# Kernel optimization log

Hardware: AMD Instinct MI355X
Metric: run time of the kernel (lower is better)

The kernel has to match this reference:

```python
import jax, jax.numpy as jnp
import numpy as np

N, E, G, H, D = 50000, 800000, 64, 2, 128  # nodes, edges, graphs, heads, out_channels
NEG_SLOPE_ATT = 0.2   # GATv2 default negative_slope
NEG_SLOPE_OUT = 0.01  # torch.nn.LeakyReLU default
BN_EPS = 1e-5


def setup_inputs() -> dict:
    key = jax.random.key(0)
    ks = jax.random.split(key, 12)
    x = jax.random.normal(ks[0], (N, 1), jnp.float32)
    edge_index = jax.random.randint(ks[1], (2, E), 0, N, dtype=jnp.int64)
    edge_attr = jax.random.normal(ks[2], (E,), jnp.float32)
    batch = jnp.sort(jax.random.randint(ks[3], (N,), 0, G, dtype=jnp.int64))
    # GATv2Conv params: lin_l/lin_r: Linear(1, H*D) with bias; lin_edge: Linear(1, H*D) no bias
    Wl = jax.random.normal(ks[4], (1, H * D), jnp.float32) * 0.5
    bl = jax.random.normal(ks[5], (H * D,), jnp.float32) * 0.1
    Wr = jax.random.normal(ks[6], (1, H * D), jnp.float32) * 0.5
    br = jax.random.normal(ks[7], (H * D,), jnp.float32) * 0.1
    We = jax.random.normal(ks[8], (1, H * D), jnp.float32) * 0.5
    att = jax.random.normal(ks[9], (H, D), jnp.float32) * 0.5
    bias = jax.random.normal(ks[10], (D,), jnp.float32) * 0.1
    gamma = jnp.ones((D,), jnp.float32)
    beta = jnp.zeros((D,), jnp.float32)
    return {"x": x, "edge_index": edge_index, "edge_attr": edge_attr, "batch": batch,
            "Wl": Wl, "bl": bl, "Wr": Wr, "br": br, "We": We, "att": att,
            "bias": bias, "gamma": gamma, "beta": beta}


def reference(x, edge_index, edge_attr, batch, Wl, bl, Wr, br, We, att, bias, gamma, beta):
    n = x.shape[0]
    src, dst = edge_index[0], edge_index[1]  # message flows src -> dst
    # node transforms: [N, H, D]
    xl = (x @ Wl + bl).reshape(n, H, D)  # lin_l (source side, also the message value)
    xr = (x @ Wr + br).reshape(n, H, D)  # lin_r (destination side)
    # edge feature embedding: [E, H, D]
    ee = (edge_attr[:, None] @ We).reshape(-1, H, D)
    # GATv2 scoring: leaky_relu(x_j + x_i + e), then dot with attention vector
    m = jax.nn.leaky_relu(xl[src] + xr[dst] + ee, NEG_SLOPE_ATT)  # [E, H, D]
    alpha = jnp.einsum('ehd,hd->eh', m, att)  # [E, H]
    # scatter-softmax over incoming edges per destination node
    amax = jax.ops.segment_max(alpha, dst, num_segments=n)  # [N, H]
    ea = jnp.exp(alpha - amax[dst])
    denom = jax.ops.segment_sum(ea, dst, num_segments=n)
    alpha = ea / (denom[dst] + 1e-16)
    # weighted scatter-add aggregation of x_j
    out = jax.ops.segment_sum(xl[src] * alpha[..., None], dst, num_segments=n)  # [N, H, D]
    out = out.mean(axis=1) + bias  # concat=False -> head average, then conv bias
    # BatchNorm1d in training mode (biased variance over nodes)
    mean = out.mean(axis=0)
    var = ((out - mean) ** 2).mean(axis=0)
    out = (out - mean) * jax.lax.rsqrt(var + BN_EPS) * gamma + beta
    out = jax.nn.leaky_relu(out, NEG_SLOPE_OUT)
    # graph-level scatter_add pooling
    return jax.ops.segment_sum(out, batch, num_segments=G)  # [G, D]
```

## Files before the change

kernel.cpp:

```cpp
#include <hip/hip_runtime.h>
#include <math.h>

#define NN 50000
#define NE 800000
#define NG 64

#define CB    1024
#define NBLK  782
#define NBUCK 196

static_assert(NBLK * CB >= NE, "chunk cover");
static_assert((NBUCK - 1) == (NN - 1) / 256, "bucket count");
static_assert(NE % 4 == 0, "edge unroll");

#define WS_C     0
#define WS_ACC   16
#define WS_BNSUM (WS_ACC + 4*NN)
#define WS_BNSQ  (WS_BNSUM + 128)
#define WS_MOM   WS_BNSUM
#define WS_EX    (WS_BNSQ + 128)
#define WS_TOT   (WS_EX + 272)
#define WS_PK    (WS_TOT + 256)
#define WS_CNT   (WS_PK + 1280)
#define WS_SORT  (WS_CNT + 256*NBLK)
#define WS_END   (WS_SORT + 4*NE)
#define WS_NEED_BYTES ((size_t)WS_END * 4 + 256)

static_assert(((WS_SORT * 4) % 16) == 0, "sort 16B alignment");

typedef float v2f __attribute__((ext_vector_type(2)));

__device__ __forceinline__ v2f pkfma(v2f a, v2f b, v2f c) {
#if __has_builtin(__builtin_elementwise_fma)
  return __builtin_elementwise_fma(a, b, c);
#else
  v2f r; r.x = fmaf(a.x, b.x, c.x); r.y = fmaf(a.y, b.y, c.y); return r;
#endif
}
__device__ __forceinline__ v2f pkabs(v2f a) {
  v2f r; r.x = fabsf(a.x); r.y = fabsf(a.y); return r;
}

#define STEP(wl_, wr_, we_, bb_, at_, xs_, xd_, ae_, acc_)                 \
  { float tt = fmaf(we_, ae_, bb_); tt = fmaf(wr_, xd_, tt);               \
    tt = fmaf(wl_, xs_, tt); acc_ = fmaf(fabsf(tt), at_, acc_); }

#define SMEM_WEIGHTS_DECL                                                  \
  __shared__ __align__(16) float sWl[256], sWr[256], sWe[256], sB[256], sAt[256];

#define SMEM_WEIGHTS_LOAD                                                  \
  { int t_ = threadIdx.x;                                                  \
    sWl[t_] = Wl[t_]; sWr[t_] = Wr[t_]; sWe[t_] = We[t_];                  \
    sB[t_] = bl[t_] + br[t_]; sAt[t_] = att[t_]; }                         \
  __syncthreads();

#define SCORES(xs_, xd_, ae_, accA, accB, out0, out1)                      \
  { float lin0 = fmaf(c0.x, xs_, fmaf(c0.y, xd_, fmaf(c0.z, ae_, c0.w))); \
    out0 = fmaf(0.4f, accA, 0.6f * lin0);                                  \
    float lin1 = fmaf(c1.x, xs_, fmaf(c1.y, xd_, fmaf(c1.z, ae_, c1.w))); \
    out1 = fmaf(0.4f, accB, 0.6f * lin1); }

#define STEP4(c, q0, q1, q2, q3)                                           \
  STEP(wl.c, wr.c, we.c, bb.c, at.c, xs0, xd0, ae0, q0)                    \
  STEP(wl.c, wr.c, we.c, bb.c, at.c, xs1, xd1, ae1, q1)                    \
  STEP(wl.c, wr.c, we.c, bb.c, at.c, xs2, xd2, ae2, q2)                    \
  STEP(wl.c, wr.c, we.c, bb.c, at.c, xs3, xd3, ae3, q3)

#define SCORE_CORE                                                         \
  int4 s4 = *(const int4*)&ei[base];                                       \
  int4 dd4 = *(const int4*)&ei[NE + base];                                 \
  float4 ae4 = *(const float4*)&eattr[base];                               \
  float xs0 = x[s4.x], xs1 = x[s4.y], xs2 = x[s4.z], xs3 = x[s4.w];        \
  float xd0 = x[dd4.x], xd1 = x[dd4.y], xd2 = x[dd4.z], xd3 = x[dd4.w];    \
  float ae0 = ae4.x, ae1 = ae4.y, ae2 = ae4.z, ae3 = ae4.w;

#define SCORE_LOOPS                                                        \
  float a00 = 0.f, a01 = 0.f, a02 = 0.f, a03 = 0.f;                        \
  float a10 = 0.f, a11 = 0.f, a12 = 0.f, a13 = 0.f;                        \
  _Pragma("unroll 2")                                                      \
  for (int j = 0; j < 128; j += 4) {                                       \
    float4 wl = *(const float4*)&sWl[j];                                   \
    float4 wr = *(const float4*)&sWr[j];                                   \
    float4 we = *(const float4*)&sWe[j];                                   \
    float4 bb = *(const float4*)&sB[j];                                    \
    float4 at = *(const float4*)&sAt[j];                                   \
    STEP4(x, a00, a01, a02, a03)                                           \
    STEP4(y, a00, a01, a02, a03)                                           \
    STEP4(z, a00, a01, a02, a03)                                           \
    STEP4(w, a00, a01, a02, a03)                                           \
  }                                                                        \
  _Pragma("unroll 2")                                                      \
  for (int j = 128; j < 256; j += 4) {                                     \
    float4 wl = *(const float4*)&sWl[j];                                   \
    float4 wr = *(const float4*)&sWr[j];                                   \
    float4 we = *(const float4*)&sWe[j];                                   \
    float4 bb = *(const float4*)&sB[j];                                    \
    float4 at = *(const float4*)&sAt[j];                                   \
    STEP4(x, a10, a11, a12, a13)                                           \
    STEP4(y, a10, a11, a12, a13)                                           \
    STEP4(z, a10, a11, a12, a13)                                           \
    STEP4(w, a10, a11, a12, a13)                                           \
  }                                                                        \
  float4 c0 = *(const float4*)&ws[WS_C];                                   \
  float4 c1 = *(const float4*)&ws[WS_C + 4];

extern "C" __global__ __launch_bounds__(256)
void k_hist(const int* __restrict__ ei,
            const float* __restrict__ att, const float* __restrict__ Wl,
            const float* __restrict__ Wr, const float* __restrict__ We,
            const float* __restrict__ bl, const float* __restrict__ br,
            float* __restrict__ ws, float* __restrict__ out)
{
  __shared__ unsigned cnt[256];
  cnt[threadIdx.x] = 0u;
  __syncthreads();
  int base = blockIdx.x * CB + (int)threadIdx.x * 4;
  if (base < NE) {
    int4 a = *(const int4*)&ei[NE + base];
    atomicAdd(&cnt[((unsigned)a.x) >> 8], 1u);
    atomicAdd(&cnt[((unsigned)a.y) >> 8], 1u);
    atomicAdd(&cnt[((unsigned)a.z) >> 8], 1u);
    atomicAdd(&cnt[((unsigned)a.w) >> 8], 1u);
  }
  __syncthreads();
  unsigned* counts = (unsigned*)(ws + WS_CNT);
  counts[(size_t)threadIdx.x * NBLK + blockIdx.x] = cnt[threadIdx.x];
  int gid = blockIdx.x * 256 + (int)threadIdx.x;
  if (gid < NG * 128) out[gid] = 0.f;
  if (gid < 14) ws[WS_MOM + gid] = 0.f;
  if (blockIdx.x == 0) {
    int t = threadIdx.x;
    int jj = (t >> 1) + ((t & 1) << 7);
    ws[WS_PK +        t] = Wl[jj];
    ws[WS_PK +  256 + t] = Wr[jj];
    ws[WS_PK +  512 + t] = We[jj];
    ws[WS_PK +  768 + t] = bl[jj] + br[jj];
    ws[WS_PK + 1024 + t] = att[jj];
    __shared__ float red[4][256];
    float a = att[t];
    red[0][t] = a * Wl[t];
    red[1][t] = a * Wr[t];
    red[2][t] = a * We[t];
    red[3][t] = a * (bl[t] + br[t]);
    __syncthreads();
    if (t < 8) {
      int k = t >> 1, h = t & 1;
      float s = 0.f;
      for (int d = 0; d < 128; ++d) s += red[k][h * 128 + d];
      ws[WS_C + h * 4 + k] = s;
    }
  }
}

extern "C" __global__ __launch_bounds__(256)
void k_scan1(float* __restrict__ ws)
{
  int b = blockIdx.x;
  int t = threadIdx.x;
  unsigned* row = (unsigned*)(ws + WS_CNT) + (size_t)b * NBLK;
  __shared__ unsigned sc[256];
  unsigned carry = 0;
  for (int c = 0; c < NBLK; c += 256) {
    int k = c + t;
    unsigned v = (k < NBLK) ? row[k] : 0u;
    sc[t] = v;
    __syncthreads();
    for (int o = 1; o < 256; o <<= 1) {
      unsigned u = (t >= o) ? sc[t - o] : 0u;
      __syncthreads();
      sc[t] += u;
      __syncthreads();
    }
    unsigned incl = sc[t];
    if (k < NBLK) row[k] = carry + incl - v;
    unsigned total = sc[255];
    __syncthreads();
    carry += total;
  }
  if (t == 0) ((unsigned*)(ws + WS_TOT))[b] = carry;
}

extern "C" __global__ __launch_bounds__(256)
void k_scan2(float* __restrict__ ws)
{
  int b = threadIdx.x;
  unsigned v = ((const unsigned*)(ws + WS_TOT))[b];
  __shared__ unsigned sc[256];
  sc[b] = v;
  __syncthreads();
  for (int o = 1; o < 256; o <<= 1) {
    unsigned u = (b >= o) ? sc[b - o] : 0u;
    __syncthreads();
    sc[b] += u;
    __syncthreads();
  }
  unsigned* ex = (unsigned*)(ws + WS_EX);
  ex[b] = sc[b] - v;
  if (b == 255) ex[256] = sc[b];
}

extern "C" __global__ __launch_bounds__(256, 2)
void k_score(const int* __restrict__ ei, const float* __restrict__ x,
             const float* __restrict__ eattr,
             const float* __restrict__ pk,
             float* __restrict__ ws)
{
  __shared__ unsigned soff[256];
  { int t_ = threadIdx.x;
    const unsigned* counts = (const unsigned*)(ws + WS_CNT);
    const unsigned* ex = (const unsigned*)(ws + WS_EX);
    soff[t_] = ex[t_] + counts[(size_t)t_ * NBLK + blockIdx.x];
  }
  __syncthreads();
  int base = blockIdx.x * CB + (int)threadIdx.x * 4;
  if (base >= NE) return;
  SCORE_CORE
  v2f A0 = {0.f, 0.f}, A1 = A0, A2 = A0, A3 = A0;
#define PKSTEP(wlp, wrp, wep, bbp, atp, xs_, xd_, ae_, acc_)               \
  { v2f tt = pkfma(wep, (v2f){ae_, ae_}, bbp);                             \
    tt = pkfma(wrp, (v2f){xd_, xd_}, tt);                                  \
    tt = pkfma(wlp, (v2f){xs_, xs_}, tt);                                  \
    acc_ = pkfma(pkabs(tt), atp, acc_); }
#define PKSTEP4(wlp, wrp, wep, bbp, atp)                                   \
  PKSTEP(wlp, wrp, wep, bbp, atp, xs0, xd0, ae0, A0)                       \
  PKSTEP(wlp, wrp, wep, bbp, atp, xs1, xd1, ae1, A1)                       \
  PKSTEP(wlp, wrp, wep, bbp, atp, xs2, xd2, ae2, A2)                       \
  PKSTEP(wlp, wrp, wep, bbp, atp, xs3, xd3, ae3, A3)
#pragma unroll 2
  for (int g = 0; g < 64; ++g) {
    float4 wl = *(const float4*)&pk[       4 * g];
    float4 wr = *(const float4*)&pk[ 256 + 4 * g];
    float4 we = *(const float4*)&pk[ 512 + 4 * g];
    float4 bb = *(const float4*)&pk[ 768 + 4 * g];
    float4 at = *(const float4*)&pk[1024 + 4 * g];
    v2f wlA = {wl.x, wl.y}, wrA = {wr.x, wr.y}, weA = {we.x, we.y};
    v2f bbA = {bb.x, bb.y}, atA = {at.x, at.y};
    v2f wlB = {wl.z, wl.w}, wrB = {wr.z, wr.w}, weB = {we.z, we.w};
    v2f bbB = {bb.z, bb.w}, atB = {at.z, at.w};
    PKSTEP4(wlA, wrA, weA, bbA, atA)
    PKSTEP4(wlB, wrB, weB, bbB, atB)
  }
#undef PKSTEP4
#undef PKSTEP
  float4 c0 = *(const float4*)&ws[WS_C];
  float4 c1 = *(const float4*)&ws[WS_C + 4];
  float4* srt = (float4*)(ws + WS_SORT);
  float s0, s1;
#define EPI(i, dv, Acc)                                                    \
  { SCORES(xs##i, xd##i, ae##i, Acc.x, Acc.y, s0, s1)                      \
    unsigned d_ = (unsigned)(dv);                                          \
    unsigned p_ = atomicAdd(&soff[d_ >> 8], 1u);                           \
    srt[p_] = make_float4(__expf(s0), __expf(s1), xs##i, __uint_as_float(d_)); }
  EPI(0, dd4.x, A0) EPI(1, dd4.y, A1)
  EPI(2, dd4.z, A2) EPI(3, dd4.w, A3)
#undef EPI
}

extern "C" __global__ __launch_bounds__(1024)
void k_gather(float* __restrict__ ws)
{
  int b = blockIdx.x;
  const int t = threadIdx.x;
  __shared__ float acc[1024];
  acc[t] = 0.f;
  __syncthreads();
  const unsigned* ex = (const unsigned*)(ws + WS_EX);
  int lo = (int)ex[b], hi = (int)ex[b + 1];
  const float4* srt = (const float4*)(ws + WS_SORT);
  for (int i = lo + t; i < hi; i += 1024) {
    float4 r = srt[i];
    int l4 = (int)(__float_as_uint(r.w) & 255u) * 4;
    atomicAdd(&acc[l4 + 0], r.x);
    atomicAdd(&acc[l4 + 1], r.y);
    atomicAdd(&acc[l4 + 2], r.x * r.z);
    atomicAdd(&acc[l4 + 3], r.y * r.z);
  }
  __syncthreads();
  float f1 = 0.f, f2 = 0.f, f3 = 0.f, f4 = 0.f;
  if (t < 256) {
    int n = (b << 8) + t;
    if (n < NN) {
      float4 A = make_float4(acc[t * 4], acc[t * 4 + 1], acc[t * 4 + 2], acc[t * 4 + 3]);
      *(float4*)&ws[WS_ACC + 4 * n] = A;
      float r0 = 1.f / (A.x + 1e-16f);
      float r1 = 1.f / (A.y + 1e-16f);
      f1 = A.x * r0; f2 = A.z * r0; f3 = A.y * r1; f4 = A.w * r1;
    }
  }
  float pm[14] = { f1, f2, f3, f4,
                   f1*f1, f1*f2, f1*f3, f1*f4,
                   f2*f2, f2*f3, f2*f4,
                   f3*f3, f3*f4, f4*f4 };
#pragma unroll
  for (int k = 0; k < 14; ++k) {
    float v = pm[k];
#pragma unroll
    for (int m = 32; m >= 1; m >>= 1) v += __shfl_xor(v, m);
    pm[k] = v;
  }
  __shared__ float smom[224];
  int wid = t >> 6, lane = t & 63;
  if (lane == 0) {
#pragma unroll
    for (int k = 0; k < 14; ++k) smom[wid * 14 + k] = pm[k];
  }
  __syncthreads();
  if (t < 14) {
    float s = 0.f;
#pragma unroll
    for (int w = 0; w < 16; ++w) s += smom[w * 14 + t];
    atomicAdd(&ws[WS_MOM + t], s);
  }
}

extern "C" __global__ __launch_bounds__(256)
void k4m_pool(const int* __restrict__ batch,
              const float* __restrict__ Wl, const float* __restrict__ bl,
              const float* __restrict__ bias, const float* __restrict__ gamma,
              const float* __restrict__ beta,
              float* __restrict__ ws, float* __restrict__ out)
{
  const int CHUNK = (NN + (int)gridDim.x - 1) / (int)gridDim.x;
  int n0 = blockIdx.x * CHUNK;
  if (n0 >= NN) return;
  int n1 = n0 + CHUNK; if (n1 > NN) n1 = NN;
  int t = threadIdx.x;
  int d = t & 127;
  int row = t >> 7;
  float S1 = ws[WS_MOM + 0], S2 = ws[WS_MOM + 1];
  float S3 = ws[WS_MOM + 2], S4 = ws[WS_MOM + 3];
  float M11 = ws[WS_MOM + 4], M12 = ws[WS_MOM + 5], M13 = ws[WS_MOM + 6];
  float M14 = ws[WS_MOM + 7], M22 = ws[WS_MOM + 8], M23 = ws[WS_MOM + 9];
  float M24 = ws[WS_MOM + 10], M33 = ws[WS_MOM + 11], M34 = ws[WS_MOM + 12];
  float M44 = ws[WS_MOM + 13];
  float g1 = 0.5f * bl[d], g2 = 0.5f * Wl[d];
  float g3 = 0.5f * bl[128 + d], g4 = 0.5f * Wl[128 + d];
  float g5 = bias[d];
  const float invN = 1.f / (float)NN;
  float dotS = g1 * S1 + g2 * S2 + g3 * S3 + g4 * S4;
  float mean = (dotS + (float)NN * g5) * invN;
  float sumsq = g1*g1*M11 + g2*g2*M22 + g3*g3*M33 + g4*g4*M44
              + 2.f*(g1*g2*M12 + g1*g3*M13 + g1*g4*M14
                   + g2*g3*M23 + g2*g4*M24 + g3*g4*M34)
              + 2.f*g5*dotS + (float)NN*g5*g5;
  float var = fmaf(sumsq, invN, -mean * mean);
  float scale = gamma[d] * rsqrtf(var + 1e-5f);
  float shift = fmaf(-mean, scale, beta[d]);
  __shared__ float pool[4][128];
  for (int i = t; i < 512; i += 256) ((float*)pool)[i] = 0.f;
  __syncthreads();
  int g0 = batch[n0];
  for (int n = n0 + row; n < n1; n += 2) {
    float4 a = *(const float4*)&ws[WS_ACC + 4 * n];
    float r0 = 1.f / (a.x + 1e-16f);
    float r1 = 1.f / (a.y + 1e-16f);
    float o = g1 * (a.x * r0) + g2 * (a.z * r0)
            + g3 * (a.y * r1) + g4 * (a.w * r1) + g5;
    float v = fmaf(o, scale, shift);
    v = v > 0.f ? v : 0.01f * v;
    int g = batch[n];
    int slot = g - g0;
    if (slot < 4) atomicAdd(&pool[slot][d], v);
    else atomicAdd(&out[g * 128 + d], v);
  }
  __syncthreads();
  for (int i = t; i < 512; i += 256) {
    int slot = i >> 7, dd = i & 127;
    int g = g0 + slot;
    float v = pool[slot][dd];
    if (g < NG && v != 0.f) atomicAdd(&out[g * 128 + dd], v);
  }
}

extern "C" __global__ __launch_bounds__(256)
void k0_init(float* __restrict__ ws,
             const float* __restrict__ att, const float* __restrict__ Wl,
             const float* __restrict__ Wr, const float* __restrict__ We,
             const float* __restrict__ bl, const float* __restrict__ br,
             float* __restrict__ out)
{
  int tid = blockIdx.x * 256 + threadIdx.x;
  int nt = gridDim.x * 256;
  for (int i = tid; i < 4 * NN; i += nt) ws[WS_ACC + i] = 0.f;
  for (int i = tid; i < 256; i += nt) ws[WS_BNSUM + i] = 0.f;
  for (int i = tid; i < NG * 128; i += nt) out[i] = 0.f;
  if (blockIdx.x == 0) {
    __shared__ float red[4][256];
    int t = threadIdx.x;
    float a = att[t];
    red[0][t] = a * Wl[t];
    red[1][t] = a * Wr[t];
    red[2][t] = a * We[t];
    red[3][t] = a * (bl[t] + br[t]);
    __syncthreads();
    if (t < 8) {
      int k = t >> 1, h = t & 1;
      float s = 0.f;
      for (int d = 0; d < 128; ++d) s += red[k][h * 128 + d];
      ws[WS_C + h * 4 + k] = s;
    }
  }
}

extern "C" __global__ __launch_bounds__(256)
void k12f(const int* __restrict__ ei, const float* __restrict__ x,
          const float* __restrict__ eattr,
          const float* __restrict__ Wl, const float* __restrict__ Wr,
          const float* __restrict__ We, const float* __restrict__ bl,
          const float* __restrict__ br, const float* __restrict__ att,
          float* __restrict__ ws)
{
  SMEM_WEIGHTS_DECL
  SMEM_WEIGHTS_LOAD
  int base = (blockIdx.x * 256 + threadIdx.x) * 4;
  if (base >= NE) return;
  SCORE_CORE
  SCORE_LOOPS
  float* acc = ws + WS_ACC;
  float s0, s1;
#define EPI2(xs_, xd_, ae_, accA, accB, dsti)                              \
  { SCORES(xs_, xd_, ae_, accA, accB, s0, s1)                              \
    float e0 = __expf(s0), e1 = __expf(s1);                                \
    float* a = &acc[4 * dsti];                                             \
    atomicAdd(a + 0, e0); atomicAdd(a + 1, e1);                            \
    atomicAdd(a + 2, e0 * xs_); atomicAdd(a + 3, e1 * xs_); }
  EPI2(xs0, xd0, ae0, a00, a10, dd4.x)
  EPI2(xs1, xd1, ae1, a01, a11, dd4.y)
  EPI2(xs2, xd2, ae2, a02, a12, dd4.z)
  EPI2(xs3, xd3, ae3, a03, a13, dd4.w)
#undef EPI2
}

__device__ __forceinline__ float node_out4(float4 a, float wl0, float wl1,
                                           float b0, float b1, float bs)
{
  float r0 = 1.f / (a.x + 1e-16f);
  float r1 = 1.f / (a.y + 1e-16f);
  return 0.5f * (fmaf(wl0, a.z * r0, b0 * (a.x * r0)) +
                 fmaf(wl1, a.w * r1, b1 * (a.y * r1))) + bs;
}

extern "C" __global__ __launch_bounds__(256)
void k3_stats(const float* __restrict__ Wl, const float* __restrict__ bl,
              const float* __restrict__ bias, float* __restrict__ ws)
{
  int d = threadIdx.x & 127;
  int row = threadIdx.x >> 7;
  float wl0 = Wl[d], wl1 = Wl[128 + d];
  float b0 = bl[d], b1 = bl[128 + d];
  float bs = bias[d];
  float sum = 0.f, sq = 0.f;
  for (int n = blockIdx.x * 2 + row; n < NN; n += gridDim.x * 2) {
    float4 a = *(const float4*)&ws[WS_ACC + 4 * n];
    float o = node_out4(a, wl0, wl1, b0, b1, bs);
    sum += o;
    sq = fmaf(o, o, sq);
  }
  __shared__ float l1[256], l2[256];
  l1[threadIdx.x] = sum; l2[threadIdx.x] = sq;
  __syncthreads();
  if (row == 0) {
    atomicAdd(&ws[WS_BNSUM + d], l1[d] + l1[128 + d]);
    atomicAdd(&ws[WS_BNSQ + d], l2[d] + l2[128 + d]);
  }
}

extern "C" __global__ __launch_bounds__(256)
void k4_pool(const int* __restrict__ batch,
             const float* __restrict__ Wl, const float* __restrict__ bl,
             const float* __restrict__ bias, const float* __restrict__ gamma,
             const float* __restrict__ beta,
             float* __restrict__ ws, float* __restrict__ out)
{
  const int CHUNK = (NN + (int)gridDim.x - 1) / (int)gridDim.x;
  int n0 = blockIdx.x * CHUNK;
  if (n0 >= NN) return;
  int n1 = n0 + CHUNK; if (n1 > NN) n1 = NN;
  int d = threadIdx.x & 127;
  int row = threadIdx.x >> 7;
  const float invN = 1.f / (float)NN;
  float mean = ws[WS_BNSUM + d] * invN;
  float var = fmaf(ws[WS_BNSQ + d], invN, -mean * mean);
  float scale = gamma[d] * rsqrtf(var + 1e-5f);
  float shift = fmaf(-mean, scale, beta[d]);
  float wl0 = Wl[d], wl1 = Wl[128 + d];
  float b0 = bl[d], b1 = bl[128 + d];
  float bs = bias[d];
  __shared__ float pool[4][128];
  for (int i = threadIdx.x; i < 512; i += 256) ((float*)pool)[i] = 0.f;
  __syncthreads();
  int g0 = batch[n0];
  for (int n = n0 + row; n < n1; n += 2) {
    float4 a = *(const float4*)&ws[WS_ACC + 4 * n];
    float o = node_out4(a, wl0, wl1, b0, b1, bs);
    float v = fmaf(o, scale, shift);
    v = v > 0.f ? v : 0.01f * v;
    int g = batch[n];
    int slot = g - g0;
    if (slot < 4) atomicAdd(&pool[slot][d], v);
    else atomicAdd(&out[g * 128 + d], v);
  }
  __syncthreads();
  for (int i = threadIdx.x; i < 512; i += 256) {
    int slot = i >> 7, dd = i & 127;
    int g = g0 + slot;
    float v = pool[slot][dd];
    if (g < NG && v != 0.f) atomicAdd(&out[g * 128 + dd], v);
  }
}

extern "C" void kernel_launch(void* const* d_in, const int* in_sizes, int n_in,
                              void* d_out, int out_size, void* d_ws, size_t ws_size,
                              hipStream_t stream) {
  const float* x     = (const float*)d_in[0];
  const int*   ei    = (const int*)d_in[1];
  const float* eattr = (const float*)d_in[2];
  const int*   batch = (const int*)d_in[3];
  const float* Wl    = (const float*)d_in[4];
  const float* bl    = (const float*)d_in[5];
  const float* Wr    = (const float*)d_in[6];
  const float* br    = (const float*)d_in[7];
  const float* We    = (const float*)d_in[8];
  const float* att   = (const float*)d_in[9];
  const float* bias  = (const float*)d_in[10];
  const float* gam   = (const float*)d_in[11];
  const float* bet   = (const float*)d_in[12];
  float* ws  = (float*)d_ws;
  float* out = (float*)d_out;

  const bool dense = (ws_size >= WS_NEED_BYTES);

  if (dense) {
    hipLaunchKernelGGL(k_hist, dim3(NBLK), dim3(256), 0, stream,
                       ei, att, Wl, Wr, We, bl, br, ws, out);
    hipLaunchKernelGGL(k_scan1, dim3(256), dim3(256), 0, stream, ws);
    hipLaunchKernelGGL(k_scan2, dim3(1), dim3(256), 0, stream, ws);
    hipLaunchKernelGGL(k_score, dim3(NBLK), dim3(256), 0, stream,
                       ei, x, eattr, (const float*)(ws + WS_PK), ws);
    hipLaunchKernelGGL(k_gather, dim3(NBUCK), dim3(1024), 0, stream, ws);
    hipLaunchKernelGGL(k4m_pool, dim3(256), dim3(256), 0, stream,
                       batch, Wl, bl, bias, gam, bet, ws, out);
  } else {
    hipLaunchKernelGGL(k0_init, dim3(128), dim3(256), 0, stream,
                       ws, att, Wl, Wr, We, bl, br, out);
    hipLaunchKernelGGL(k12f, dim3((NE / 4 + 255) / 256), dim3(256), 0, stream,
                       ei, x, eattr, Wl, Wr, We, bl, br, att, ws);
    hipLaunchKernelGGL(k3_stats, dim3(256), dim3(256), 0, stream,
                       Wl, bl, bias, ws);
    hipLaunchKernelGGL(k4_pool, dim3(256), dim3(256), 0, stream,
                       batch, Wl, bl, bias, gam, bet, ws, out);
  }
}
```

Baseline: 190.8 us.

## Fuse dense pipeline into single cooperative persistent kernel with grid syncs

```diff
diff --git a/kernel.cpp b/kernel.cpp
--- a/kernel.cpp
+++ b/kernel.cpp
@@ -1,5 +1,8 @@
 #include <hip/hip_runtime.h>
+#include <hip/hip_cooperative_groups.h>
 #include <math.h>
+
+namespace cg = cooperative_groups;
 
 #define NN 50000
 #define NE 800000
@@ -9,9 +12,16 @@
 #define NBLK  782
 #define NBUCK 196
 
+#define GB    256
+#define GT    1024
+#define CBM   4096
+#define NSBM  196
+
 static_assert(NBLK * CB >= NE, "chunk cover");
 static_assert((NBUCK - 1) == (NN - 1) / 256, "bucket count");
 static_assert(NE % 4 == 0, "edge unroll");
+static_assert(NSBM * CBM >= NE, "mega cover");
+static_assert(NSBM <= GB, "mega blocks");
 
 #define WS_C     0
 #define WS_ACC   16
@@ -104,6 +114,250 @@
   float4 c0 = *(const float4*)&ws[WS_C];                                   \
   float4 c1 = *(const float4*)&ws[WS_C + 4];
 
+extern "C" __global__ __launch_bounds__(1024, 4)
+void k_mega(const int* __restrict__ ei, const float* __restrict__ x,
+            const float* __restrict__ eattr, const int* __restrict__ batch,
+            const float* __restrict__ Wl, const float* __restrict__ bl,
+            const float* __restrict__ Wr, const float* __restrict__ br,
+            const float* __restrict__ We, const float* __restrict__ att,
+            const float* __restrict__ bias, const float* __restrict__ gamma,
+            const float* __restrict__ beta,
+            float* __restrict__ ws, float* __restrict__ out)
+{
+  cg::grid_group grid = cg::this_grid();
+  const int b = blockIdx.x;
+  const int t = threadIdx.x;
+  unsigned* counts = (unsigned*)(ws + WS_CNT);
+  unsigned* ex = (unsigned*)(ws + WS_EX);
+  unsigned* tot = (unsigned*)(ws + WS_TOT);
+
+  __shared__ unsigned cnt[256];
+  __shared__ unsigned sc[256];
+  __shared__ float acc[1024];
+  __shared__ float smom[224];
+  __shared__ float redc[4][256];
+  __shared__ float pool[4][128];
+
+  if (t < 256) cnt[t] = 0u;
+  int gid = b * GT + t;
+  if (gid < NG * 128) out[gid] = 0.f;
+  if (gid < 14) ws[WS_MOM + gid] = 0.f;
+  if (b == 0 && t < 256) {
+    int jj = (t >> 1) + ((t & 1) << 7);
+    ws[WS_PK +        t] = Wl[jj];
+    ws[WS_PK +  256 + t] = Wr[jj];
+    ws[WS_PK +  512 + t] = We[jj];
+    ws[WS_PK +  768 + t] = bl[jj] + br[jj];
+    ws[WS_PK + 1024 + t] = att[jj];
+    float a = att[t];
+    redc[0][t] = a * Wl[t];
+    redc[1][t] = a * Wr[t];
+    redc[2][t] = a * We[t];
+    redc[3][t] = a * (bl[t] + br[t]);
+  }
+  __syncthreads();
+  if (b == 0 && t < 8) {
+    int k = t >> 1, h = t & 1;
+    float s = 0.f;
+    for (int d = 0; d < 128; ++d) s += redc[k][h * 128 + d];
+    ws[WS_C + h * 4 + k] = s;
+  }
+  const int base = gid * 4;
+  if (base < NE) {
+    int4 a4 = *(const int4*)&ei[NE + base];
+    atomicAdd(&cnt[((unsigned)a4.x) >> 8], 1u);
+    atomicAdd(&cnt[((unsigned)a4.y) >> 8], 1u);
+    atomicAdd(&cnt[((unsigned)a4.z) >> 8], 1u);
+    atomicAdd(&cnt[((unsigned)a4.w) >> 8], 1u);
+  }
+  __syncthreads();
+  if (t < 256) counts[(size_t)t * 256 + b] = cnt[t];
+  grid.sync();
+
+  {
+    unsigned v = 0, incl = 0;
+    unsigned* row = counts + (size_t)b * 256;
+    if (t < 256) { v = row[t]; sc[t] = v; }
+    __syncthreads();
+    for (int o = 1; o < 256; o <<= 1) {
+      unsigned u = (t < 256 && t >= o) ? sc[t - o] : 0u;
+      __syncthreads();
+      if (t < 256) sc[t] += u;
+      __syncthreads();
+    }
+    if (t < 256) { incl = sc[t]; row[t] = incl - v; }
+    if (t == 255) tot[b] = incl;
+  }
+  grid.sync();
+
+  if (b == 0) {
+    unsigned v = 0;
+    if (t < 256) { v = tot[t]; sc[t] = v; }
+    __syncthreads();
+    for (int o = 1; o < 256; o <<= 1) {
+      unsigned u = (t < 256 && t >= o) ? sc[t - o] : 0u;
+      __syncthreads();
+      if (t < 256) sc[t] += u;
+      __syncthreads();
+    }
+    if (t < 256) ex[t] = sc[t] - v;
+    if (t == 255) ex[256] = sc[255];
+  }
+  grid.sync();
+
+  {
+    if (t < 256) sc[t] = ex[t] + counts[(size_t)t * 256 + b];
+    __syncthreads();
+    if (base < NE) {
+      SCORE_CORE
+      const float* pk = ws + WS_PK;
+      v2f A0 = {0.f, 0.f}, A1 = A0, A2 = A0, A3 = A0;
+#define PKSTEP(wlp, wrp, wep, bbp, atp, xs_, xd_, ae_, acc_)               \
+      { v2f tt = pkfma(wep, (v2f){ae_, ae_}, bbp);                         \
+        tt = pkfma(wrp, (v2f){xd_, xd_}, tt);                              \
+        tt = pkfma(wlp, (v2f){xs_, xs_}, tt);                              \
+        acc_ = pkfma(pkabs(tt), atp, acc_); }
+#define PKSTEP4(wlp, wrp, wep, bbp, atp)                                   \
+      PKSTEP(wlp, wrp, wep, bbp, atp, xs0, xd0, ae0, A0)                   \
+      PKSTEP(wlp, wrp, wep, bbp, atp, xs1, xd1, ae1, A1)                   \
+      PKSTEP(wlp, wrp, wep, bbp, atp, xs2, xd2, ae2, A2)                   \
+      PKSTEP(wlp, wrp, wep, bbp, atp, xs3, xd3, ae3, A3)
+#pragma unroll 2
+      for (int g = 0; g < 64; ++g) {
+        float4 wl = *(const float4*)&pk[       4 * g];
+        float4 wr = *(const float4*)&pk[ 256 + 4 * g];
+        float4 we = *(const float4*)&pk[ 512 + 4 * g];
+        float4 bb = *(const float4*)&pk[ 768 + 4 * g];
+        float4 at = *(const float4*)&pk[1024 + 4 * g];
+        v2f wlA = {wl.x, wl.y}, wrA = {wr.x, wr.y}, weA = {we.x, we.y};
+        v2f bbA = {bb.x, bb.y}, atA = {at.x, at.y};
+        v2f wlB = {wl.z, wl.w}, wrB = {wr.z, wr.w}, weB = {we.z, we.w};
+        v2f bbB = {bb.z, bb.w}, atB = {at.z, at.w};
+        PKSTEP4(wlA, wrA, weA, bbA, atA)
+        PKSTEP4(wlB, wrB, weB, bbB, atB)
+      }
+#undef PKSTEP4
+#undef PKSTEP
+      float4 c0 = *(const float4*)&ws[WS_C];
+      float4 c1 = *(const float4*)&ws[WS_C + 4];
+      float4* srt = (float4*)(ws + WS_SORT);
+      float s0, s1;
+#define EPIM(i, dv, Acc)                                                   \
+      { SCORES(xs##i, xd##i, ae##i, Acc.x, Acc.y, s0, s1)                  \
+        unsigned d_ = (unsigned)(dv);                                      \
+        unsigned p_ = atomicAdd(&sc[d_ >> 8], 1u);                         \
+        srt[p_] = make_float4(__expf(s0), __expf(s1), xs##i, __uint_as_float(d_)); }
+      EPIM(0, dd4.x, A0) EPIM(1, dd4.y, A1)
+      EPIM(2, dd4.z, A2) EPIM(3, dd4.w, A3)
+#undef EPIM
+    }
+  }
+  grid.sync();
+
+  if (b < NBUCK) {
+    acc[t] = 0.f;
+    __syncthreads();
+    int lo = (int)ex[b], hi = (int)ex[b + 1];
+    const float4* srt = (const float4*)(ws + WS_SORT);
+    for (int i = lo + t; i < hi; i += GT) {
+      float4 r = srt[i];
+      int l4 = (int)(__float_as_uint(r.w) & 255u) * 4;
+      atomicAdd(&acc[l4 + 0], r.x);
+      atomicAdd(&acc[l4 + 1], r.y);
+      atomicAdd(&acc[l4 + 2], r.x * r.z);
+      atomicAdd(&acc[l4 + 3], r.y * r.z);
+    }
+    __syncthreads();
+    float f1 = 0.f, f2 = 0.f, f3 = 0.f, f4 = 0.f;
+    if (t < 256) {
+      int n = (b << 8) + t;
+      if (n < NN) {
+        float4 A = make_float4(acc[t * 4], acc[t * 4 + 1], acc[t * 4 + 2], acc[t * 4 + 3]);
+        *(float4*)&ws[WS_ACC + 4 * n] = A;
+        float r0 = 1.f / (A.x + 1e-16f);
+        float r1 = 1.f / (A.y + 1e-16f);
+        f1 = A.x * r0; f2 = A.z * r0; f3 = A.y * r1; f4 = A.w * r1;
+      }
+    }
+    float pm[14] = { f1, f2, f3, f4,
+                     f1*f1, f1*f2, f1*f3, f1*f4,
+                     f2*f2, f2*f3, f2*f4,
+                     f3*f3, f3*f4, f4*f4 };
+#pragma unroll
+    for (int k = 0; k < 14; ++k) {
+      float v = pm[k];
+#pragma unroll
+      for (int m = 32; m >= 1; m >>= 1) v += __shfl_xor(v, m);
+      pm[k] = v;
+    }
+    int wid = t >> 6, lane = t & 63;
+    if (lane == 0) {
+#pragma unroll
+      for (int k = 0; k < 14; ++k) smom[wid * 14 + k] = pm[k];
+    }
+    __syncthreads();
+    if (t < 14) {
+      float s = 0.f;
+#pragma unroll
+      for (int w = 0; w < 16; ++w) s += smom[w * 14 + t];
+      atomicAdd(&ws[WS_MOM + t], s);
+    }
+  }
+  grid.sync();
+
+  {
+    const int CHUNK = (NN + GB - 1) / GB;
+    int n0 = b * CHUNK;
+    int n1 = n0 + CHUNK; if (n1 > NN) n1 = NN;
+    int d = t & 127;
+    int row = t >> 7;
+    float S1 = ws[WS_MOM + 0], S2 = ws[WS_MOM + 1];
+    float S3 = ws[WS_MOM + 2], S4 = ws[WS_MOM + 3];
+    float M11 = ws[WS_MOM + 4], M12 = ws[WS_MOM + 5], M13 = ws[WS_MOM + 6];
+    float M14 = ws[WS_MOM + 7], M22 = ws[WS_MOM + 8], M23 = ws[WS_MOM + 9];
+    float M24 = ws[WS_MOM + 10], M33 = ws[WS_MOM + 11], M34 = ws[WS_MOM + 12];
+    float M44 = ws[WS_MOM + 13];
+    float g1 = 0.5f * bl[d], g2 = 0.5f * Wl[d];
+    float g3 = 0.5f * bl[128 + d], g4 = 0.5f * Wl[128 + d];
+    float g5 = bias[d];
+    const float invN = 1.f / (float)NN;
+    float dotS = g1 * S1 + g2 * S2 + g3 * S3 + g4 * S4;
+    float mean = (dotS + (float)NN * g5) * invN;
+    float sumsq = g1*g1*M11 + g2*g2*M22 + g3*g3*M33 + g4*g4*M44
+                + 2.f*(g1*g2*M12 + g1*g3*M13 + g1*g4*M14
+                     + g2*g3*M23 + g2*g4*M24 + g3*g4*M34)
+                + 2.f*g5*dotS + (float)NN*g5*g5;
+    float var = fmaf(sumsq, invN, -mean * mean);
+    float scale = gamma[d] * rsqrtf(var + 1e-5f);
+    float shift = fmaf(-mean, scale, beta[d]);
+    if (t < 512) ((float*)pool)[t] = 0.f;
+    __syncthreads();
+    if (n0 < NN) {
+      int g0 = batch[n0];
+      for (int n = n0 + row; n < n1; n += 8) {
+        float4 a = *(const float4*)&ws[WS_ACC + 4 * n];
+        float r0 = 1.f / (a.x + 1e-16f);
+        float r1 = 1.f / (a.y + 1e-16f);
+        float o = g1 * (a.x * r0) + g2 * (a.z * r0)
+                + g3 * (a.y * r1) + g4 * (a.w * r1) + g5;
+        float v = fmaf(o, scale, shift);
+        v = v > 0.f ? v : 0.01f * v;
+        int g = batch[n];
+        int slot = g - g0;
+        if (slot < 4) atomicAdd(&pool[slot][d], v);
+        else atomicAdd(&out[g * 128 + d], v);
+      }
+      __syncthreads();
+      if (t < 512) {
+        int slot = t >> 7, dd = t & 127;
+        int g = g0 + slot;
+        float v = pool[slot][dd];
+        if (g < NG && v != 0.f) atomicAdd(&out[g * 128 + dd], v);
+      }
+    }
+  }
+}
+
 extern "C" __global__ __launch_bounds__(256)
 void k_hist(const int* __restrict__ ei,
             const float* __restrict__ att, const float* __restrict__ Wl,
@@ -531,6 +785,15 @@
   const bool dense = (ws_size >= WS_NEED_BYTES);
 
   if (dense) {
+    void* args[] = { (void*)&ei, (void*)&x, (void*)&eattr, (void*)&batch,
+                     (void*)&Wl, (void*)&bl, (void*)&Wr, (void*)&br,
+                     (void*)&We, (void*)&att, (void*)&bias, (void*)&gam,
+                     (void*)&bet, (void*)&ws, (void*)&out };
+    hipError_t err = hipLaunchCooperativeKernel((const void*)k_mega,
+                                                dim3(GB), dim3(GT),
+                                                args, 0, stream);
+    if (err == hipSuccess) return;
+    (void)hipGetLastError();
     hipLaunchKernelGGL(k_hist, dim3(NBLK), dim3(256), 0, stream,
                        ei, att, Wl, Wr, We, bl, br, ws, out);
     hipLaunchKernelGGL(k_scan1, dim3(256), dim3(256), 0, stream, ws);
```

Result: slower. 357.5 us (+87.3%).
